# Performance work log

Hardware: AMD Instinct MI355X
Metric: run time of the kernel (lower is better)

Reference implementation:

```python
import jax, jax.numpy as jnp
import numpy as np

NEG_BIG = -1.0e9  # matches tf's -1000000000.0 masking constant


def setup_inputs() -> dict:
    key = jax.random.key(0)
    k0, k1, k2 = jax.random.split(key, 3)
    B, T, F, U = 32, 2048, 512, 128
    x = jax.random.normal(k0, (B, T, F), dtype=jnp.float32)
    W1 = jax.random.normal(k1, (F, U), dtype=jnp.float32) * 0.05
    b1 = jnp.zeros((U,), dtype=jnp.float32)
    W2 = jax.random.normal(k2, (U, 1), dtype=jnp.float32) * 0.05
    b2 = jnp.zeros((1,), dtype=jnp.float32)
    return {"x": x, "W1": W1, "b1": b1, "W2": W2, "b2": b2, "k": 64}


def reference(x, W1, b1, W2, b2, k):
    # x: [B, T, F]
    # padding mask: frame is valid if any feature is nonzero
    mask = jnp.any(x != 0, axis=-1, keepdims=True).astype(x.dtype)  # [B, T, 1]
    # policy MLP scoring
    h = jax.nn.relu(jnp.einsum('btf,fu->btu', x, W1) + b1)          # [B, T, U]
    scores = jnp.einsum('btu,uo->bto', h, W2) + b2                  # [B, T, 1]
    scores = scores * mask + NEG_BIG * (1.0 - mask)
    # top-k frame selection (inference path, training=None)
    _, top_idx = jax.lax.top_k(jnp.squeeze(scores, axis=-1), k)     # [B, k]
    B, T = x.shape[0], x.shape[1]
    sel = jnp.zeros((B, T), dtype=x.dtype)
    # tf.scatter_nd adds; top-k indices are unique per row so add == set
    sel = sel.at[jnp.arange(B)[:, None], top_idx].add(1.0)          # [B, T]
    return x * sel[:, :, None]
```

## Files before the change

### kernel.cpp

```cpp
#include <hip/hip_runtime.h>
#include <stddef.h>

constexpr int B = 32;
constexpr int T = 2048;
constexpr int F = 512;
constexpr int U = 128;
constexpr float NEG_BIG = -1.0e9f;

typedef __attribute__((ext_vector_type(8))) short short8;
typedef __attribute__((ext_vector_type(4))) float f32x4;
typedef __attribute__((ext_vector_type(4))) unsigned short u16x4;

__device__ __forceinline__ unsigned short f2bf(float f) {
    unsigned int u = __float_as_uint(f);
    u += 0x7FFFu + ((u >> 16) & 1u);
    return (unsigned short)(u >> 16);
}
__device__ __forceinline__ float bf2f(unsigned short h) {
    return __uint_as_float(((unsigned int)h) << 16);
}

__global__ __launch_bounds__(256) void prep_w(
    const float* __restrict__ W1,
    unsigned short* __restrict__ WThi,
    unsigned short* __restrict__ WTlo)
{
    const int idx = blockIdx.x * 256 + threadIdx.x;
    const int k = idx >> 7;
    const int u = idx & 127;
    const float w = W1[idx];
    const unsigned short hi = f2bf(w);
    const unsigned short lo = f2bf(w - bf2f(hi));
    WThi[(size_t)u * F + k] = hi;
    WTlo[(size_t)u * F + k] = lo;
}

constexpr int LDK = 40;

__global__ __launch_bounds__(256) void score_kernel(
    const float* __restrict__ x,
    const unsigned short* __restrict__ WThi,
    const unsigned short* __restrict__ WTlo,
    const float* __restrict__ b1,
    const float* __restrict__ W2,
    const float* __restrict__ b2,
    float* __restrict__ scores)
{
    __shared__ __align__(16) unsigned short xs_hi[64 * LDK];
    __shared__ __align__(16) unsigned short xs_lo[64 * LDK];
    __shared__ __align__(16) unsigned short wt_hi[U * LDK];
    __shared__ __align__(16) unsigned short wt_lo[U * LDK];
    __shared__ unsigned nz[64];
    __shared__ float partial[64][4];

    const int tid  = threadIdx.x;
    const int wid  = tid >> 6;
    const int lane = tid & 63;
    const int l15  = lane & 15;
    const int g    = lane >> 4;
    const int m0   = blockIdx.x * 64;

    if (tid < 64) nz[tid] = 0u;

    float b1v[2], w2v[2];
#pragma unroll
    for (int j = 0; j < 2; ++j) {
        const int u = (2 * wid + j) * 16 + l15;
        b1v[j] = b1[u];
        w2v[j] = W2[u];
    }

    f32x4 acc[4][2] = {};

    __syncthreads();

    for (int k0 = 0; k0 < F; k0 += 32) {
#pragma unroll
        for (int r = 0; r < 2; ++r) {
            const int q  = tid + r * 256;
            const int fr = q >> 3;
            const int kk = (q & 7) * 4;
            const float4 v = *reinterpret_cast<const float4*>(
                &x[(size_t)(m0 + fr) * F + k0 + kk]);
            u16x4 hv, lv;
            hv.x = f2bf(v.x); hv.y = f2bf(v.y); hv.z = f2bf(v.z); hv.w = f2bf(v.w);
            lv.x = f2bf(v.x - bf2f(hv.x));
            lv.y = f2bf(v.y - bf2f(hv.y));
            lv.z = f2bf(v.z - bf2f(hv.z));
            lv.w = f2bf(v.w - bf2f(hv.w));
            *reinterpret_cast<u16x4*>(&xs_hi[fr * LDK + kk]) = hv;
            *reinterpret_cast<u16x4*>(&xs_lo[fr * LDK + kk]) = lv;
            if (v.x != 0.0f || v.y != 0.0f || v.z != 0.0f || v.w != 0.0f)
                nz[fr] = 1u;
        }
        {
            const int n    = tid >> 1;
            const int half = tid & 1;
            const float4* sh = reinterpret_cast<const float4*>(
                WThi + (size_t)n * F + k0 + half * 16);
            const float4* sl = reinterpret_cast<const float4*>(
                WTlo + (size_t)n * F + k0 + half * 16);
            float4* dh = reinterpret_cast<float4*>(&wt_hi[n * LDK + half * 16]);
            float4* dl = reinterpret_cast<float4*>(&wt_lo[n * LDK + half * 16]);
            dh[0] = sh[0]; dh[1] = sh[1];
            dl[0] = sl[0]; dl[1] = sl[1];
        }
        __syncthreads();

        short8 bh[2], bl[2];
#pragma unroll
        for (int j = 0; j < 2; ++j) {
            const int n = (2 * wid + j) * 16 + l15;
            bh[j] = *reinterpret_cast<const short8*>(&wt_hi[n * LDK + g * 8]);
            bl[j] = *reinterpret_cast<const short8*>(&wt_lo[n * LDK + g * 8]);
        }
#pragma unroll
        for (int mf = 0; mf < 4; ++mf) {
            const short8 ah = *reinterpret_cast<const short8*>(
                &xs_hi[(mf * 16 + l15) * LDK + g * 8]);
            const short8 al = *reinterpret_cast<const short8*>(
                &xs_lo[(mf * 16 + l15) * LDK + g * 8]);
#pragma unroll
            for (int j = 0; j < 2; ++j) {
                acc[mf][j] = __builtin_amdgcn_mfma_f32_16x16x32_bf16(ah, bh[j], acc[mf][j], 0, 0, 0);
                acc[mf][j] = __builtin_amdgcn_mfma_f32_16x16x32_bf16(ah, bl[j], acc[mf][j], 0, 0, 0);
                acc[mf][j] = __builtin_amdgcn_mfma_f32_16x16x32_bf16(al, bh[j], acc[mf][j], 0, 0, 0);
            }
        }
        __syncthreads();
    }

#pragma unroll
    for (int mf = 0; mf < 4; ++mf) {
#pragma unroll
        for (int r = 0; r < 4; ++r) {
            float s = 0.0f;
#pragma unroll
            for (int j = 0; j < 2; ++j) {
                float h = acc[mf][j][r] + b1v[j];
                h = h > 0.0f ? h : 0.0f;
                s += h * w2v[j];
            }
            s += __shfl_xor(s, 1);
            s += __shfl_xor(s, 2);
            s += __shfl_xor(s, 4);
            s += __shfl_xor(s, 8);
            if (l15 == 0) partial[mf * 16 + g * 4 + r][wid] = s;
        }
    }
    __syncthreads();

    if (tid < 64) {
        const float s = partial[tid][0] + partial[tid][1] +
                        partial[tid][2] + partial[tid][3] + b2[0];
        scores[m0 + tid] = nz[tid] ? s : NEG_BIG;
    }
}

__global__ __launch_bounds__(256) void topk_kernel(
    const float* __restrict__ scores,
    const int* __restrict__ kp,
    int* __restrict__ sel)
{
    __shared__ float srow[T];

    const int b     = blockIdx.x >> 3;
    const int chunk = blockIdx.x & 7;
    const float* row = scores + (size_t)b * T;

    for (int i = threadIdx.x; i < T / 4; i += 256)
        reinterpret_cast<float4*>(srow)[i] =
            reinterpret_cast<const float4*>(row)[i];
    __syncthreads();

    const int t   = chunk * 256 + threadIdx.x;
    const float s = srow[t];
    int cnt = 0;
    for (int i = 0; i < T / 4; ++i) {
        const float4 v = reinterpret_cast<const float4*>(srow)[i];
        const int base = i * 4;
        cnt += (v.x > s) || (v.x == s && (base + 0) < t);
        cnt += (v.y > s) || (v.y == s && (base + 1) < t);
        cnt += (v.z > s) || (v.z == s && (base + 2) < t);
        cnt += (v.w > s) || (v.w == s && (base + 3) < t);
    }
    const int k = kp[0];
    sel[(size_t)b * T + t] = (cnt < k) ? 1 : 0;
}

__global__ __launch_bounds__(256) void out_kernel(
    const float* __restrict__ x,
    const int* __restrict__ sel,
    float* __restrict__ out)
{
    const size_t total  = (size_t)B * T * (F / 4);
    const size_t stride = (size_t)gridDim.x * blockDim.x;
    for (size_t idx = (size_t)blockIdx.x * blockDim.x + threadIdx.x;
         idx < total; idx += stride) {
        const size_t frame = idx >> 7;
        float4 v = make_float4(0.0f, 0.0f, 0.0f, 0.0f);
        if (sel[frame])
            v = reinterpret_cast<const float4*>(x)[idx];
        reinterpret_cast<float4*>(out)[idx] = v;
    }
}

extern "C" void kernel_launch(void* const* d_in, const int* in_sizes, int n_in,
                              void* d_out, int out_size, void* d_ws, size_t ws_size,
                              hipStream_t stream)
{
    const float* x  = (const float*)d_in[0];
    const float* W1 = (const float*)d_in[1];
    const float* b1 = (const float*)d_in[2];
    const float* W2 = (const float*)d_in[3];
    const float* b2 = (const float*)d_in[4];
    const int*   kp = (const int*)d_in[5];

    char* ws = (char*)d_ws;
    unsigned short* WThi = (unsigned short*)ws;
    unsigned short* WTlo = (unsigned short*)(ws + 131072);
    float* scores        = (float*)(ws + 262144);
    int*   sel           = (int*)(ws + 524288);

    float* out = (float*)d_out;

    prep_w<<<256, 256, 0, stream>>>(W1, WThi, WTlo);
    score_kernel<<<(B * T) / 64, 256, 0, stream>>>(x, WThi, WTlo, b1, W2, b2, scores);
    topk_kernel<<<B * 8, 256, 0, stream>>>(scores, kp, sel);
    out_kernel<<<4096, 256, 0, stream>>>(x, sel, out);
}
```

Baseline: 128.4 us.

## Drop LDS staging in score GEMM and fuse top-k with output masking

The score kernel now has each wave compute a full 16-row by 128-unit tile, loading x and the split-bf16 weights straight from global memory into MFMA operands. This removes the shared-memory staging, the barriers and the cross-wave partial reduction, and uses a ballot for the nonzero-frame mask. The top-k selection kernel is fused with the output-masking kernel, so selection flags stay in shared memory and one kernel launch plus the sel buffer round trip go away. In exchange, W1 is re-read from global or L2 by every wave without reuse, and the fused output pass runs on only 256 blocks, which may underuse bandwidth.

```diff
diff --git a/kernel.cpp b/kernel.cpp
--- a/kernel.cpp
+++ b/kernel.cpp
@@ -9,7 +9,6 @@
 
 typedef __attribute__((ext_vector_type(8))) short short8;
 typedef __attribute__((ext_vector_type(4))) float f32x4;
-typedef __attribute__((ext_vector_type(4))) unsigned short u16x4;
 
 __device__ __forceinline__ unsigned short f2bf(float f) {
     unsigned int u = __float_as_uint(f);
@@ -35,8 +34,6 @@
     WTlo[(size_t)u * F + k] = lo;
 }
 
-constexpr int LDK = 40;
-
 __global__ __launch_bounds__(256) void score_kernel(
     const float* __restrict__ x,
     const unsigned short* __restrict__ WThi,
@@ -46,123 +43,85 @@
     const float* __restrict__ b2,
     float* __restrict__ scores)
 {
-    __shared__ __align__(16) unsigned short xs_hi[64 * LDK];
-    __shared__ __align__(16) unsigned short xs_lo[64 * LDK];
-    __shared__ __align__(16) unsigned short wt_hi[U * LDK];
-    __shared__ __align__(16) unsigned short wt_lo[U * LDK];
-    __shared__ unsigned nz[64];
-    __shared__ float partial[64][4];
-
     const int tid  = threadIdx.x;
     const int wid  = tid >> 6;
     const int lane = tid & 63;
     const int l15  = lane & 15;
     const int g    = lane >> 4;
-    const int m0   = blockIdx.x * 64;
+    const int m0   = blockIdx.x * 64 + wid * 16;
 
-    if (tid < 64) nz[tid] = 0u;
+    const float* xrow = x + (size_t)(m0 + l15) * F + g * 8;
+    const unsigned short* whr = WThi + (size_t)l15 * F + g * 8;
+    const unsigned short* wlr = WTlo + (size_t)l15 * F + g * 8;
 
-    float b1v[2], w2v[2];
+    f32x4 acc[8] = {};
+    bool nzflag = false;
+
+#pragma unroll 2
+    for (int k0 = 0; k0 < F; k0 += 32) {
+        const float4 a0 = *reinterpret_cast<const float4*>(xrow + k0);
+        const float4 a1 = *reinterpret_cast<const float4*>(xrow + k0 + 4);
+        const float av[8] = { a0.x, a0.y, a0.z, a0.w, a1.x, a1.y, a1.z, a1.w };
+        short8 ah, al;
 #pragma unroll
-    for (int j = 0; j < 2; ++j) {
-        const int u = (2 * wid + j) * 16 + l15;
-        b1v[j] = b1[u];
-        w2v[j] = W2[u];
+        for (int j = 0; j < 8; ++j) {
+            const unsigned short hi = f2bf(av[j]);
+            ah[j] = (short)hi;
+            al[j] = (short)f2bf(av[j] - bf2f(hi));
+            nzflag |= (av[j] != 0.0f);
+        }
+#pragma unroll
+        for (int nf = 0; nf < 8; ++nf) {
+            const short8 bh = *reinterpret_cast<const short8*>(
+                whr + (size_t)(nf * 16) * F + k0);
+            const short8 bl = *reinterpret_cast<const short8*>(
+                wlr + (size_t)(nf * 16) * F + k0);
+            acc[nf] = __builtin_amdgcn_mfma_f32_16x16x32_bf16(ah, bh, acc[nf], 0, 0, 0);
+            acc[nf] = __builtin_amdgcn_mfma_f32_16x16x32_bf16(ah, bl, acc[nf], 0, 0, 0);
+            acc[nf] = __builtin_amdgcn_mfma_f32_16x16x32_bf16(al, bh, acc[nf], 0, 0, 0);
+        }
     }
 
-    f32x4 acc[4][2] = {};
+    const unsigned long long nzb = __ballot(nzflag);
 
-    __syncthreads();
-
-    for (int k0 = 0; k0 < F; k0 += 32) {
+    float b1v[8], w2v[8];
 #pragma unroll
-        for (int r = 0; r < 2; ++r) {
-            const int q  = tid + r * 256;
-            const int fr = q >> 3;
-            const int kk = (q & 7) * 4;
-            const float4 v = *reinterpret_cast<const float4*>(
-                &x[(size_t)(m0 + fr) * F + k0 + kk]);
-            u16x4 hv, lv;
-            hv.x = f2bf(v.x); hv.y = f2bf(v.y); hv.z = f2bf(v.z); hv.w = f2bf(v.w);
-            lv.x = f2bf(v.x - bf2f(hv.x));
-            lv.y = f2bf(v.y - bf2f(hv.y));
-            lv.z = f2bf(v.z - bf2f(hv.z));
-            lv.w = f2bf(v.w - bf2f(hv.w));
-            *reinterpret_cast<u16x4*>(&xs_hi[fr * LDK + kk]) = hv;
-            *reinterpret_cast<u16x4*>(&xs_lo[fr * LDK + kk]) = lv;
-            if (v.x != 0.0f || v.y != 0.0f || v.z != 0.0f || v.w != 0.0f)
-                nz[fr] = 1u;
-        }
-        {
-            const int n    = tid >> 1;
-            const int half = tid & 1;
-            const float4* sh = reinterpret_cast<const float4*>(
-                WThi + (size_t)n * F + k0 + half * 16);
-            const float4* sl = reinterpret_cast<const float4*>(
-                WTlo + (size_t)n * F + k0 + half * 16);
-            float4* dh = reinterpret_cast<float4*>(&wt_hi[n * LDK + half * 16]);
-            float4* dl = reinterpret_cast<float4*>(&wt_lo[n * LDK + half * 16]);
-            dh[0] = sh[0]; dh[1] = sh[1];
-            dl[0] = sl[0]; dl[1] = sl[1];
-        }
-        __syncthreads();
-
-        short8 bh[2], bl[2];
-#pragma unroll
-        for (int j = 0; j < 2; ++j) {
-            const int n = (2 * wid + j) * 16 + l15;
-            bh[j] = *reinterpret_cast<const short8*>(&wt_hi[n * LDK + g * 8]);
-            bl[j] = *reinterpret_cast<const short8*>(&wt_lo[n * LDK + g * 8]);
-        }
-#pragma unroll
-        for (int mf = 0; mf < 4; ++mf) {
-            const short8 ah = *reinterpret_cast<const short8*>(
-                &xs_hi[(mf * 16 + l15) * LDK + g * 8]);
-            const short8 al = *reinterpret_cast<const short8*>(
-                &xs_lo[(mf * 16 + l15) * LDK + g * 8]);
-#pragma unroll
-            for (int j = 0; j < 2; ++j) {
-                acc[mf][j] = __builtin_amdgcn_mfma_f32_16x16x32_bf16(ah, bh[j], acc[mf][j], 0, 0, 0);
-                acc[mf][j] = __builtin_amdgcn_mfma_f32_16x16x32_bf16(ah, bl[j], acc[mf][j], 0, 0, 0);
-                acc[mf][j] = __builtin_amdgcn_mfma_f32_16x16x32_bf16(al, bh[j], acc[mf][j], 0, 0, 0);
-            }
-        }
-        __syncthreads();
+    for (int nf = 0; nf < 8; ++nf) {
+        const int u = nf * 16 + l15;
+        b1v[nf] = b1[u];
+        w2v[nf] = W2[u];
     }
+    const float bias2 = b2[0];
 
 #pragma unroll
-    for (int mf = 0; mf < 4; ++mf) {
+    for (int r = 0; r < 4; ++r) {
+        float s = 0.0f;
 #pragma unroll
-        for (int r = 0; r < 4; ++r) {
-            float s = 0.0f;
-#pragma unroll
-            for (int j = 0; j < 2; ++j) {
-                float h = acc[mf][j][r] + b1v[j];
-                h = h > 0.0f ? h : 0.0f;
-                s += h * w2v[j];
-            }
-            s += __shfl_xor(s, 1);
-            s += __shfl_xor(s, 2);
-            s += __shfl_xor(s, 4);
-            s += __shfl_xor(s, 8);
-            if (l15 == 0) partial[mf * 16 + g * 4 + r][wid] = s;
+        for (int nf = 0; nf < 8; ++nf) {
+            float h = acc[nf][r] + b1v[nf];
+            h = h > 0.0f ? h : 0.0f;
+            s += h * w2v[nf];
         }
-    }
-    __syncthreads();
-
-    if (tid < 64) {
-        const float s = partial[tid][0] + partial[tid][1] +
-                        partial[tid][2] + partial[tid][3] + b2[0];
-        scores[m0 + tid] = nz[tid] ? s : NEG_BIG;
+        s += __shfl_xor(s, 1);
+        s += __shfl_xor(s, 2);
+        s += __shfl_xor(s, 4);
+        s += __shfl_xor(s, 8);
+        if (l15 == 0) {
+            const int fr = g * 4 + r;
+            const bool nz = (nzb & (0x0001000100010001ULL << fr)) != 0ULL;
+            scores[m0 + fr] = nz ? (s + bias2) : NEG_BIG;
+        }
     }
 }
 
-__global__ __launch_bounds__(256) void topk_kernel(
+__global__ __launch_bounds__(256) void topk_out_kernel(
     const float* __restrict__ scores,
     const int* __restrict__ kp,
-    int* __restrict__ sel)
+    const float* __restrict__ x,
+    float* __restrict__ out)
 {
     __shared__ float srow[T];
+    __shared__ int ssel[256];
 
     const int b     = blockIdx.x >> 3;
     const int chunk = blockIdx.x & 7;
@@ -184,24 +143,21 @@
         cnt += (v.z > s) || (v.z == s && (base + 2) < t);
         cnt += (v.w > s) || (v.w == s && (base + 3) < t);
     }
-    const int k = kp[0];
-    sel[(size_t)b * T + t] = (cnt < k) ? 1 : 0;
-}
+    ssel[threadIdx.x] = (cnt < kp[0]) ? 1 : 0;
+    __syncthreads();
 
-__global__ __launch_bounds__(256) void out_kernel(
-    const float* __restrict__ x,
-    const int* __restrict__ sel,
-    float* __restrict__ out)
-{
-    const size_t total  = (size_t)B * T * (F / 4);
-    const size_t stride = (size_t)gridDim.x * blockDim.x;
-    for (size_t idx = (size_t)blockIdx.x * blockDim.x + threadIdx.x;
-         idx < total; idx += stride) {
-        const size_t frame = idx >> 7;
-        float4 v = make_float4(0.0f, 0.0f, 0.0f, 0.0f);
-        if (sel[frame])
-            v = reinterpret_cast<const float4*>(x)[idx];
-        reinterpret_cast<float4*>(out)[idx] = v;
+    const size_t base4 = ((size_t)b * T + (size_t)chunk * 256) * (F / 4);
+    const float4* x4 = reinterpret_cast<const float4*>(x) + base4;
+    float4*       o4 = reinterpret_cast<float4*>(out) + base4;
+    const float4 z = make_float4(0.0f, 0.0f, 0.0f, 0.0f);
+
+#pragma unroll 4
+    for (int it = 0; it < 128; ++it) {
+        const int q  = it * 256 + threadIdx.x;
+        const int fr = q >> 7;
+        float4 v = z;
+        if (ssel[fr]) v = x4[q];
+        o4[q] = v;
     }
 }
 
@@ -220,12 +176,10 @@
     unsigned short* WThi = (unsigned short*)ws;
     unsigned short* WTlo = (unsigned short*)(ws + 131072);
     float* scores        = (float*)(ws + 262144);
-    int*   sel           = (int*)(ws + 524288);
 
     float* out = (float*)d_out;
 
     prep_w<<<256, 256, 0, stream>>>(W1, WThi, WTlo);
     score_kernel<<<(B * T) / 64, 256, 0, stream>>>(x, WThi, WTlo, b1, W2, b2, scores);
-    topk_kernel<<<B * 8, 256, 0, stream>>>(scores, kp, sel);
-    out_kernel<<<4096, 256, 0, stream>>>(x, sel, out);
+    topk_out_kernel<<<B * 8, 256, 0, stream>>>(scores, kp, x, out);
 }
```

Measured after the change: 213.4 us. 66.2% more time.
